# Kernel tuning notes

Measured on AMD Instinct MI355X. Metric: run time of the kernel, lower is better.

Reference implementation:

```python
import jax, jax.numpy as jnp
import numpy as np

N = 65536      # total nodes
D = 256        # score_dim
E = 128        # embed_dim
H = 8          # num_heads
HID = 256      # MLP hidden width
G = 128        # number of graphs (segments)


def setup_inputs() -> dict:
    key = jax.random.key(0)
    ks = jax.random.split(key, 16)
    w = lambda k, shape, s=0.02: jax.random.normal(k, shape, jnp.float32) * s
    return {
        "score_matrix": jax.random.normal(ks[0], (N, D), jnp.float32),
        "x": jax.random.normal(ks[1], (N, D), jnp.float32),  # unused by forward (as in source)
        "batch": jnp.sort(jax.random.randint(ks[2], (N,), 0, G)),
        "pos": jax.random.normal(ks[3], (1, D), jnp.float32),
        "para": jax.random.normal(ks[4], (1, E), jnp.float32),
        # stacked per-head MLP weights (q, k, v): in_dim->256->embed_dim
        "Wq1": w(ks[5], (H, D, HID)), "bq1": jnp.zeros((H, HID), jnp.float32),
        "Wq2": w(ks[6], (H, HID, E)), "bq2": jnp.zeros((H, E), jnp.float32),
        "Wk1": w(ks[7], (H, D, HID)), "bk1": jnp.zeros((H, HID), jnp.float32),
        "Wk2": w(ks[8], (H, HID, E)), "bk2": jnp.zeros((H, E), jnp.float32),
        "Wv1": w(ks[9], (H, D, HID)), "bv1": jnp.zeros((H, HID), jnp.float32),
        "Wv2": w(ks[10], (H, HID, E)), "bv2": jnp.zeros((H, E), jnp.float32),
        # out MLP: (H*E)->256->E
        "Wo1": w(ks[11], (H * E, HID)), "bo1": jnp.zeros((HID,), jnp.float32),
        "Wo2": w(ks[12], (HID, E)), "bo2": jnp.zeros((E,), jnp.float32),
    }


def _head_mlp(xs, W1, b1, W2, b2):
    # xs: [N, D]; W1: [H, D, HID]; W2: [H, HID, E] -> [N, H, E]
    h = jax.nn.relu(jnp.einsum('nd,hdk->nhk', xs, W1) + b1)
    return jnp.einsum('nhk,hke->nhe', h, W2) + b2


def _segment_softmax(src, idx, num_seg):
    # grouped softmax along axis 0 (matches torch scatter_max/scatter_add version)
    m = jax.ops.segment_max(src, idx, num_segments=num_seg)
    ex = jnp.exp(src - m[idx])
    den = jax.ops.segment_sum(ex, idx, num_segments=num_seg)[idx] + 1e-16
    return ex / den


def reference(score_matrix, x, batch, pos, para,
              Wq1, bq1, Wq2, bq2, Wk1, bk1, Wk2, bk2, Wv1, bv1, Wv2, bv2,
              Wo1, bo1, Wo2, bo2):
    sm = score_matrix + pos                                  # [N, D]
    q = _head_mlp(sm, Wq1, bq1, Wq2, bq2)                    # [N, H, E]
    k = _head_mlp(sm, Wk1, bk1, Wk2, bk2)                    # [N, H, E]
    v = _head_mlp(sm, Wv1, bv1, Wv2, bv2)                    # [N, H, E]
    scores = jnp.einsum('nhe,nge->nhg', q, k) / np.float32(np.sqrt(E))  # [N, H, H]
    aw = _segment_softmax(scores, batch, G)                  # [N, H, H]
    s = jnp.einsum('nhg,nge->nhe', aw, v).reshape(sm.shape[0], H * E)   # [N, H*E]
    out = jax.nn.relu(s @ Wo1 + bo1) @ Wo2 + bo2             # [N, E]
    return out + para
```

## Files before the change

kernel.cpp:

```cpp
#include <hip/hip_runtime.h>

#define N_NODES 65536
#define NSEG    128

using s16x8 = __attribute__((ext_vector_type(8))) short;
using s16x4 = __attribute__((ext_vector_type(4))) short;
using f32x4 = __attribute__((ext_vector_type(4))) float;

__device__ __forceinline__ float bf2f(unsigned short s) {
    union { unsigned u; float f; } x; x.u = ((unsigned)s) << 16; return x.f;
}
__device__ __forceinline__ short f2bf(float f) {
    union { float f; unsigned u; } x; x.f = f;
    unsigned r = x.u + 0x7FFFu + ((x.u >> 16) & 1u);
    return (short)(r >> 16);
}
__device__ __forceinline__ void gload_lds16(const void* g, void* lds) {
    __builtin_amdgcn_global_load_lds((const __attribute__((address_space(1))) void*)g,
                                     (__attribute__((address_space(3))) void*)lds, 16, 0, 0);
}


__global__ void prep_sm_kernel(const float* __restrict__ score, const float* __restrict__ pos,
                               short* __restrict__ sm) {
    int i = blockIdx.x * blockDim.x + threadIdx.x;
    int base = i * 4;
    f32x4 s = __builtin_nontemporal_load((const f32x4*)(score + base));
    f32x4 p = *(const f32x4*)(pos + (base & 255));
    s16x4 o;
#pragma unroll
    for (int j = 0; j < 4; ++j) o[j] = f2bf(s[j] + p[j]);
    *(s16x4*)(sm + base) = o;
}

__global__ void transpose_all_kernel(const float* __restrict__ Wq1, const float* __restrict__ Wk1,
                                     const float* __restrict__ Wv1, const float* __restrict__ Wq2,
                                     const float* __restrict__ Wk2, const float* __restrict__ Wv2,
                                     const float* __restrict__ Wo1, const float* __restrict__ Wo2,
                                     short* __restrict__ W1T, short* __restrict__ W2T,
                                     short* __restrict__ Wo1T, short* __restrict__ Wo2T) {
    int t = blockIdx.x;
    const float* in; short* out; int R, C, tx, ty;
    if (t < 1536) {
        int u = t >> 6, rem = t & 63;
        const float* s = (u < 8) ? Wq1 : (u < 16) ? Wk1 : Wv1;
        in = s + (long)(u & 7) * 65536; out = W1T + (long)u * 65536;
        R = 256; C = 256; tx = rem & 7; ty = rem >> 3;
    } else if (t < 2304) {
        int t2 = t - 1536, u = t2 >> 5, rem = t2 & 31;
        const float* s = (u < 8) ? Wq2 : (u < 16) ? Wk2 : Wv2;
        in = s + (long)(u & 7) * 32768; out = W2T + (long)u * 32768;
        R = 256; C = 128; tx = rem & 3; ty = rem >> 2;
    } else if (t < 2560) {
        int t3 = t - 2304;
        in = Wo1; out = Wo1T; R = 1024; C = 256; tx = t3 & 7; ty = t3 >> 3;
    } else {
        int t4 = t - 2560;
        in = Wo2; out = Wo2T; R = 256; C = 128; tx = t4 & 3; ty = t4 >> 2;
    }
    __shared__ float tbuf[32][33];
    const int c0 = tx * 32, r0 = ty * 32;
    const int lx = threadIdx.x & 31, ly = threadIdx.x >> 5;
#pragma unroll
    for (int i = 0; i < 32; i += 8)
        tbuf[ly + i][lx] = in[(long)(r0 + ly + i) * C + c0 + lx];
    __syncthreads();
#pragma unroll
    for (int i = 0; i < 32; i += 8)
        out[(long)(c0 + ly + i) * R + r0 + lx] = f2bf(tbuf[lx][ly + i]);
}

__global__ void prep_small_kernel(const float* __restrict__ bq1, const float* __restrict__ bk1,
                                  const float* __restrict__ bv1, const float* __restrict__ bq2,
                                  const float* __restrict__ bk2, const float* __restrict__ bv2,
                                  const float* __restrict__ bo2, const float* __restrict__ para,
                                  float* __restrict__ b1cat, float* __restrict__ b2cat,
                                  float* __restrict__ bo2p) {
    int i = blockIdx.x * blockDim.x + threadIdx.x;
    if (i < 6144) {
        int u = i >> 8, j = i & 255;
        const float* s = (u < 8) ? (bq1 + u * 256 + j)
                       : (u < 16) ? (bk1 + (u - 8) * 256 + j)
                                  : (bv1 + (u - 16) * 256 + j);
        b1cat[i] = *s;
    } else if (i < 9216) {
        int ii = i - 6144;
        int u = ii >> 7, j = ii & 127;
        const float* s = (u < 8) ? (bq2 + u * 128 + j)
                       : (u < 16) ? (bk2 + (u - 8) * 128 + j)
                                  : (bv2 + (u - 16) * 128 + j);
        b2cat[ii] = *s;
    } else if (i < 9344) {
        int e = i - 9216;
        bo2p[e] = bo2[e] + para[e];
    }
}

template <bool OUTBF16>
__global__ __launch_bounds__(512, 2)
void fused_mlp(const short* __restrict__ A, int lda,
               const short* __restrict__ B1, long b1_ustride,
               const float* __restrict__ bias1, int bias1_ustride,
               const short* __restrict__ B2, long b2_ustride,
               const float* __restrict__ bias2, int bias2_ustride,
               void* __restrict__ Cv, int ldc, long c_ustride, int K1) {
    const int u = blockIdx.y;
    B1    += (long)u * b1_ustride;
    bias1 += (long)u * bias1_ustride;
    B2    += (long)u * b2_ustride;
    bias2 += (long)u * bias2_ustride;

    __shared__ __align__(16) short lds[24576];
    short* Bs = lds;
    short* As = lds + 8192;
    short* hs = lds + 8192;

    const int tid = threadIdx.x, lane = tid & 63, wave = tid >> 6;
    const int wm = wave >> 2;
    const int wn = wave & 3;
    const int brow = blockIdx.x * 128;

    const int lrow = lane >> 3;
    const int schk = ((lane & 7) ^ lrow) * 8;
    const int nkt1 = K1 >> 6;
    const int l15 = lane & 15, lq = lane >> 4;

    f32x4 acc2[4][2];
#pragma unroll
    for (int i = 0; i < 4; ++i)
#pragma unroll
        for (int j = 0; j < 2; ++j) acc2[i][j] = (f32x4){0.f, 0.f, 0.f, 0.f};

    for (int p = 0; p < 2; ++p) {
        f32x4 acc1[4][2];
#pragma unroll
        for (int i = 0; i < 4; ++i)
#pragma unroll
            for (int j = 0; j < 2; ++j) acc1[i][j] = (f32x4){0.f, 0.f, 0.f, 0.f};

        for (int kt = 0; kt < nkt1; ++kt) {
            __syncthreads();
            const int ko = kt * 64;
#pragma unroll
            for (int i = 0; i < 2; ++i) {
                int cch = wave * 2 + i;
                int r = cch * 8 + lrow;
                gload_lds16(A  + (long)(brow + r) * lda + ko + schk, &As[cch * 512]);
                gload_lds16(B1 + (long)(p * 128 + r) * K1 + ko + schk, &Bs[cch * 512]);
            }
            __syncthreads();
#pragma unroll
            for (int kk = 0; kk < 2; ++kk) {
                const int slot = (((kk * 4) + lq) ^ (lane & 7)) * 8;
                s16x8 af[4], bfv[2];
#pragma unroll
                for (int i = 0; i < 4; ++i)
                    af[i] = *(const s16x8*)&As[(wm * 64 + i * 16 + l15) * 64 + slot];
#pragma unroll
                for (int j = 0; j < 2; ++j)
                    bfv[j] = *(const s16x8*)&Bs[(wn * 32 + j * 16 + l15) * 64 + slot];
#pragma unroll
                for (int i = 0; i < 4; ++i)
#pragma unroll
                    for (int j = 0; j < 2; ++j)
                        acc1[i][j] = __builtin_amdgcn_mfma_f32_16x16x32_bf16(bfv[j], af[i], acc1[i][j], 0, 0, 0);
            }
        }

        __syncthreads();

#pragma unroll
        for (int i = 0; i < 2; ++i) {
            int cch = wave * 2 + i;
            int r = cch * 8 + lrow;
            gload_lds16(B2 + (long)r * 256 + p * 128 + schk, &Bs[cch * 512]);
        }

        {
            const int cbq = lq << 2;
#pragma unroll
            for (int j = 0; j < 2; ++j) {
                int cb = wn * 32 + j * 16 + cbq;
                f32x4 bv = *(const f32x4*)(bias1 + p * 128 + cb);
#pragma unroll
                for (int i = 0; i < 4; ++i) {
                    int node = wm * 64 + i * 16 + l15;
                    s16x4 hv;
#pragma unroll
                    for (int r = 0; r < 4; ++r)
                        hv[r] = f2bf(fmaxf(acc1[i][j][r] + bv[r], 0.f));
                    *(s16x4*)&hs[node * 128 + (((cb >> 3) ^ (node & 7)) << 3) + (cb & 7)] = hv;
                }
            }
        }

#pragma unroll
        for (int kt2 = 0; kt2 < 2; ++kt2) {
            __syncthreads();
#pragma unroll
            for (int kk = 0; kk < 2; ++kk) {
                const int slotb = (((kk * 4) + lq) ^ (lane & 7)) * 8;
                s16x8 hf[4], wf[2];
#pragma unroll
                for (int i = 0; i < 4; ++i) {
                    int row = wm * 64 + i * 16 + l15;
                    int c = kt2 * 8 + kk * 4 + lq;
                    hf[i] = *(const s16x8*)&hs[row * 128 + ((c ^ (row & 7)) << 3)];
                }
#pragma unroll
                for (int j = 0; j < 2; ++j)
                    wf[j] = *(const s16x8*)&Bs[(wn * 32 + j * 16 + l15) * 64 + slotb];
#pragma unroll
                for (int i = 0; i < 4; ++i)
#pragma unroll
                    for (int j = 0; j < 2; ++j)
                        acc2[i][j] = __builtin_amdgcn_mfma_f32_16x16x32_bf16(wf[j], hf[i], acc2[i][j], 0, 0, 0);
            }
            if (kt2 == 0) {
                __syncthreads();
#pragma unroll
                for (int i = 0; i < 2; ++i) {
                    int cch = wave * 2 + i;
                    int r = cch * 8 + lrow;
                    gload_lds16(B2 + (long)r * 256 + p * 128 + 64 + schk, &Bs[cch * 512]);
                }
            }
        }
    }

    const int cbq = lq << 2;
    if (OUTBF16) {
        __syncthreads();
        short* Cs = hs;
#pragma unroll
        for (int j = 0; j < 2; ++j) {
            int cb = wn * 32 + j * 16 + cbq;
            f32x4 bv = *(const f32x4*)(bias2 + cb);
#pragma unroll
            for (int i = 0; i < 4; ++i) {
                int node = wm * 64 + i * 16 + l15;
                s16x4 ov;
#pragma unroll
                for (int r = 0; r < 4; ++r) ov[r] = f2bf(acc2[i][j][r] + bv[r]);
                *(s16x4*)&Cs[node * 128 + (((cb >> 3) ^ (node & 7)) << 3) + (cb & 7)] = ov;
            }
        }
        __syncthreads();
        short* cbase = (short*)Cv + u * c_ustride + (long)brow * ldc;
#pragma unroll
        for (int p8 = 0; p8 < 4; ++p8) {
            int g = tid + p8 * 512;
            int row = g >> 4, ck = g & 15;
            s16x8 val = *(const s16x8*)&Cs[row * 128 + ((ck ^ (row & 7)) * 8)];
            *(s16x8*)(cbase + (long)row * ldc + ck * 8) = val;
        }
    } else {
        float* cbase = (float*)Cv + u * c_ustride;
#pragma unroll
        for (int j = 0; j < 2; ++j) {
            int cb = wn * 32 + j * 16 + cbq;
            f32x4 bv = *(const f32x4*)(bias2 + cb);
#pragma unroll
            for (int i = 0; i < 4; ++i) {
                int node = wm * 64 + i * 16 + l15;
                f32x4 o;
#pragma unroll
                for (int r = 0; r < 4; ++r) o[r] = acc2[i][j][r] + bv[r];
                *(f32x4*)&cbase[(long)(brow + node) * ldc + cb] = o;
            }
        }
    }
}

__global__ __launch_bounds__(512, 2)
void fused_mlp2(const short* __restrict__ A, int lda,
                const short* __restrict__ B1,
                const float* __restrict__ bias1,
                const short* __restrict__ B2,
                const float* __restrict__ bias2,
                short* __restrict__ Cv, int ldc) {
    const int u = blockIdx.y;
    B1    += (long)u * 65536;
    bias1 += u * 256;
    B2    += (long)u * 32768;
    bias2 += u * 128;

    __shared__ __align__(16) short lds[24576];
    short* Ws  = lds;
    short* Bp0 = lds + 8192;
    short* Bp1 = lds + 16384;
    short* hs  = lds + 8192;

    const int tid = threadIdx.x, lane = tid & 63, wave = tid >> 6;
    const int wm = wave >> 2, wn = wave & 3;
    const int brow = blockIdx.x * 128;
    const int lrow = lane >> 3;
    const int schk = ((lane & 7) ^ lrow) * 8;
    const int l15 = lane & 15, lq = lane >> 4;
    const int cch0 = wave * 2, cch1 = cch0 + 1;
    const int ar0 = cch0 * 8 + lrow, ar1 = cch1 * 8 + lrow;

    f32x4 acc1[2][4][2];
    f32x4 acc2[4][2];
#pragma unroll
    for (int i = 0; i < 4; ++i)
#pragma unroll
        for (int j = 0; j < 2; ++j) {
            acc1[0][i][j] = (f32x4){0.f, 0.f, 0.f, 0.f};
            acc1[1][i][j] = (f32x4){0.f, 0.f, 0.f, 0.f};
            acc2[i][j]    = (f32x4){0.f, 0.f, 0.f, 0.f};
        }

    for (int kt = 0; kt < 4; ++kt) {
        __syncthreads();
        const int ko = kt * 64;
        gload_lds16(A + (long)(brow + ar0) * lda + ko + schk, &Ws[cch0 * 512]);
        gload_lds16(A + (long)(brow + ar1) * lda + ko + schk, &Ws[cch1 * 512]);
        gload_lds16(B1 + (long)ar0 * 256 + ko + schk, &Bp0[cch0 * 512]);
        gload_lds16(B1 + (long)ar1 * 256 + ko + schk, &Bp0[cch1 * 512]);
        gload_lds16(B1 + (long)(128 + ar0) * 256 + ko + schk, &Bp1[cch0 * 512]);
        gload_lds16(B1 + (long)(128 + ar1) * 256 + ko + schk, &Bp1[cch1 * 512]);
        __syncthreads();
#pragma unroll
        for (int kk = 0; kk < 2; ++kk) {
            const int slot = (((kk * 4) + lq) ^ (lane & 7)) * 8;
            s16x8 af[4], b0[2], b1v[2];
#pragma unroll
            for (int i = 0; i < 4; ++i)
                af[i] = *(const s16x8*)&Ws[(wm * 64 + i * 16 + l15) * 64 + slot];
#pragma unroll
            for (int j = 0; j < 2; ++j) {
                b0[j]  = *(const s16x8*)&Bp0[(wn * 32 + j * 16 + l15) * 64 + slot];
                b1v[j] = *(const s16x8*)&Bp1[(wn * 32 + j * 16 + l15) * 64 + slot];
            }
#pragma unroll
            for (int i = 0; i < 4; ++i)
#pragma unroll
                for (int j = 0; j < 2; ++j) {
                    acc1[0][i][j] = __builtin_amdgcn_mfma_f32_16x16x32_bf16(b0[j],  af[i], acc1[0][i][j], 0, 0, 0);
                    acc1[1][i][j] = __builtin_amdgcn_mfma_f32_16x16x32_bf16(b1v[j], af[i], acc1[1][i][j], 0, 0, 0);
                }
        }
    }

    __syncthreads();

    const int cbq = lq << 2;
#pragma unroll
    for (int p = 0; p < 2; ++p) {
        gload_lds16(B2 + (long)ar0 * 256 + p * 128 + schk, &Ws[cch0 * 512]);
        gload_lds16(B2 + (long)ar1 * 256 + p * 128 + schk, &Ws[cch1 * 512]);

#pragma unroll
        for (int j = 0; j < 2; ++j) {
            int cb = wn * 32 + j * 16 + cbq;
            f32x4 bv = *(const f32x4*)(bias1 + p * 128 + cb);
#pragma unroll
            for (int i = 0; i < 4; ++i) {
                int node = wm * 64 + i * 16 + l15;
                s16x4 hv;
#pragma unroll
                for (int r = 0; r < 4; ++r)
                    hv[r] = f2bf(fmaxf(acc1[p][i][j][r] + bv[r], 0.f));
                *(s16x4*)&hs[node * 128 + (((cb >> 3) ^ (node & 7)) << 3) + (cb & 7)] = hv;
            }
        }
        __syncthreads();

#pragma unroll
        for (int kt2 = 0; kt2 < 2; ++kt2) {
#pragma unroll
            for (int kk = 0; kk < 2; ++kk) {
                const int slotb = (((kk * 4) + lq) ^ (lane & 7)) * 8;
                s16x8 hf[4], wf[2];
#pragma unroll
                for (int i = 0; i < 4; ++i) {
                    int row = wm * 64 + i * 16 + l15;
                    int c = kt2 * 8 + kk * 4 + lq;
                    hf[i] = *(const s16x8*)&hs[row * 128 + ((c ^ (row & 7)) << 3)];
                }
#pragma unroll
                for (int j = 0; j < 2; ++j)
                    wf[j] = *(const s16x8*)&Ws[(wn * 32 + j * 16 + l15) * 64 + slotb];
#pragma unroll
                for (int i = 0; i < 4; ++i)
#pragma unroll
                    for (int j = 0; j < 2; ++j)
                        acc2[i][j] = __builtin_amdgcn_mfma_f32_16x16x32_bf16(wf[j], hf[i], acc2[i][j], 0, 0, 0);
            }
            if (kt2 == 0) {
                __syncthreads();
                gload_lds16(B2 + (long)ar0 * 256 + p * 128 + 64 + schk, &Ws[cch0 * 512]);
                gload_lds16(B2 + (long)ar1 * 256 + p * 128 + 64 + schk, &Ws[cch1 * 512]);
                __syncthreads();
            }
        }
        __syncthreads();
    }

    short* Cs = hs;
#pragma unroll
    for (int j = 0; j < 2; ++j) {
        int cb = wn * 32 + j * 16 + cbq;
        f32x4 bv = *(const f32x4*)(bias2 + cb);
#pragma unroll
        for (int i = 0; i < 4; ++i) {
            int node = wm * 64 + i * 16 + l15;
            s16x4 ov;
#pragma unroll
            for (int r = 0; r < 4; ++r) ov[r] = f2bf(acc2[i][j][r] + bv[r]);
            *(s16x4*)&Cs[node * 128 + (((cb >> 3) ^ (node & 7)) << 3) + (cb & 7)] = ov;
        }
    }
    __syncthreads();
    short* cbase = Cv + (long)u * 128 + (long)brow * ldc;
#pragma unroll
    for (int p8 = 0; p8 < 4; ++p8) {
        int g = tid + p8 * 512;
        int row = g >> 4, ck = g & 15;
        s16x8 val = *(const s16x8*)&Cs[row * 128 + ((ck ^ (row & 7)) * 8)];
        *(s16x8*)(cbase + (long)row * ldc + ck * 8) = val;
    }
}


__global__ void scores_mfma_kernel(const short* __restrict__ qk, float* __restrict__ scores,
                                   int nc) {
    const int lane = threadIdx.x & 63;
    int gw = (blockIdx.x * blockDim.x + threadIdx.x) >> 6;
    int nw = (gridDim.x * blockDim.x) >> 6;
    const int npairs = nc >> 1;
    const int r = lane & 15, ks = lane >> 4;
    for (int p = gw; p < npairs; p += nw) {
        const long n0 = (long)p * 2;
        const short* qp = qk + (n0 + (r >> 3)) * 2048 + (r & 7) * 128 + ks * 8;
        const short* kp = qp + 1024;
        f32x4 acc = (f32x4){0.f, 0.f, 0.f, 0.f};
#pragma unroll
        for (int kt = 0; kt < 4; ++kt) {
            s16x8 a = *(const s16x8*)(qp + kt * 32);
            s16x8 b = *(const s16x8*)(kp + kt * 32);
            acc = __builtin_amdgcn_mfma_f32_16x16x32_bf16(a, b, acc, 0, 0, 0);
        }
        const int c = lane & 15, rr0 = (lane >> 4) * 4;
        if ((rr0 >> 3) == (c >> 3)) {
            float* o = scores + (n0 + (rr0 >> 3)) * 64 + (c & 7);
#pragma unroll
            for (int reg = 0; reg < 4; ++reg)
                o[((rr0 & 7) + reg) * 8] = acc[reg] * 0.08838834764831845f;
        }
    }
}

__global__ void segstats1_kernel(const float* __restrict__ scores, const int* __restrict__ batch,
                                 float* __restrict__ pm, float* __restrict__ ps) {
    const int g = blockIdx.x, sl = blockIdx.y;
    int lo = 0, hi = N_NODES;
    while (lo < hi) { int mid = (lo + hi) >> 1; if (batch[mid] < g) lo = mid + 1; else hi = mid; }
    const int start = lo;
    hi = N_NODES;
    while (lo < hi) { int mid = (lo + hi) >> 1; if (batch[mid] <= g) lo = mid + 1; else hi = mid; }
    const int end = lo;
    const int len = end - start;
    const int s0 = start + (len * sl) / 8;
    const int s1 = start + (len * (sl + 1)) / 8;

    const int e = threadIdx.x & 63, sub = threadIdx.x >> 6;
    __shared__ float red[4][64];
    float m = -1e30f;
    for (int n = s0 + sub; n < s1; n += 4)
        m = fmaxf(m, scores[(long)n * 64 + e]);
    red[sub][e] = m;
    __syncthreads();
    m = fmaxf(fmaxf(red[0][e], red[1][e]), fmaxf(red[2][e], red[3][e]));
    __syncthreads();
    float s = 0.f;
    for (int n = s0 + sub; n < s1; n += 4)
        s += expf(scores[(long)n * 64 + e] - m);
    red[sub][e] = s;
    __syncthreads();
    if (sub == 0) {
        int idx = (g * 8 + sl) * 64 + e;
        pm[idx] = m;
        ps[idx] = red[0][e] + red[1][e] + red[2][e] + red[3][e];
    }
}

__global__ void segstats2_kernel(const float* __restrict__ pm, const float* __restrict__ ps,
                                 float* __restrict__ segm, float* __restrict__ segdinv) {
    const int g = blockIdx.x, e = threadIdx.x;
    float M = -1e30f;
#pragma unroll
    for (int sl = 0; sl < 8; ++sl)
        M = fmaxf(M, pm[(g * 8 + sl) * 64 + e]);
    float den = 1e-16f;
#pragma unroll
    for (int sl = 0; sl < 8; ++sl) {
        int idx = (g * 8 + sl) * 64 + e;
        den += ps[idx] * expf(pm[idx] - M);
    }
    segm[g * 64 + e]    = M;
    segdinv[g * 64 + e] = 1.f / den;
}

__global__ void pv_kernel(const short* __restrict__ v, short* __restrict__ sout,
                          const float* __restrict__ scores, const int* __restrict__ batch,
                          const float* __restrict__ segm, const float* __restrict__ segdinv,
                          int n0) {
    __shared__ float aw[16][64];
    const int t = threadIdx.x;
    const int nodeL0 = blockIdx.x * 16;
    {
        int j0 = t * 4;
        int nl = j0 >> 6, e0 = j0 & 63;
        int n = n0 + nodeL0 + nl;
        int b = batch[n];
        f32x4 sc = *(const f32x4*)(scores + (long)n * 64 + e0);
#pragma unroll
        for (int i = 0; i < 4; ++i)
            aw[nl][e0 + i] = expf(sc[i] - segm[b * 64 + e0 + i]) * segdinv[b * 64 + e0 + i];
    }
    __syncthreads();
    const int nl = t >> 4;
    const int ec = (t & 15) * 8;
    const long nloc = nodeL0 + nl;
    const short* vp = v + nloc * 1024 + ec;
    float acc[8][8];
#pragma unroll
    for (int h = 0; h < 8; ++h)
#pragma unroll
        for (int j = 0; j < 8; ++j) acc[h][j] = 0.f;
#pragma unroll
    for (int g = 0; g < 8; ++g) {
        s16x8 vv = *(const s16x8*)(vp + g * 128);
        float vf[8];
#pragma unroll
        for (int j = 0; j < 8; ++j) vf[j] = bf2f((unsigned short)vv[j]);
#pragma unroll
        for (int h = 0; h < 8; ++h) {
            float wgt = aw[nl][h * 8 + g];
#pragma unroll
            for (int j = 0; j < 8; ++j) acc[h][j] += wgt * vf[j];
        }
    }
#pragma unroll
    for (int h = 0; h < 8; ++h) {
        s16x8 o;
#pragma unroll
        for (int j = 0; j < 8; ++j) o[j] = f2bf(acc[h][j]);
        *(s16x8*)(sout + nloc * 1024 + h * 128 + ec) = o;
    }
}


extern "C" void kernel_launch(void* const* d_in, const int* in_sizes, int n_in,
                              void* d_out, int out_size, void* d_ws, size_t ws_size,
                              hipStream_t stream) {
    const float* score = (const float*)d_in[0];
    const int*   batch = (const int*)d_in[2];
    const float* pos   = (const float*)d_in[3];
    const float* para  = (const float*)d_in[4];
    const float* Wq1 = (const float*)d_in[5];
    const float* bq1 = (const float*)d_in[6];
    const float* Wq2 = (const float*)d_in[7];
    const float* bq2 = (const float*)d_in[8];
    const float* Wk1 = (const float*)d_in[9];
    const float* bk1 = (const float*)d_in[10];
    const float* Wk2 = (const float*)d_in[11];
    const float* bk2 = (const float*)d_in[12];
    const float* Wv1 = (const float*)d_in[13];
    const float* bv1 = (const float*)d_in[14];
    const float* Wv2 = (const float*)d_in[15];
    const float* bv2 = (const float*)d_in[16];
    const float* Wo1 = (const float*)d_in[17];
    const float* bo1 = (const float*)d_in[18];
    const float* Wo2 = (const float*)d_in[19];
    const float* bo2 = (const float*)d_in[20];
    float* out = (float*)d_out;
    (void)in_sizes; (void)n_in; (void)out_size;

    char* w = (char*)d_ws;
    short* sm     = (short*)w; w += (size_t)N_NODES * 256 * 2;
    float* scoresb= (float*)w; w += (size_t)N_NODES * 64 * 4;
    short* W1T    = (short*)w; w += (size_t)24 * 256 * 256 * 2;
    short* W2T    = (short*)w; w += (size_t)24 * 128 * 256 * 2;
    short* Wo1T   = (short*)w; w += (size_t)256 * 1024 * 2;
    short* Wo2T   = (short*)w; w += (size_t)128 * 256 * 2;
    float* b1cat  = (float*)w; w += 6144 * 4;
    float* b2cat  = (float*)w; w += 3072 * 4;
    float* bo2p   = (float*)w; w += 1024;
    float* segm   = (float*)w; w += 8192 * 4;
    float* segdi  = (float*)w; w += 8192 * 4;
    float* pm     = (float*)w; w += 65536 * 4;
    float* ps     = (float*)w; w += 65536 * 4;
    size_t persist = (size_t)(w - (char*)d_ws);
    size_t area = ws_size - persist;

    int NC = 32768;
    while (NC > 1024 && (size_t)NC * 4096 > area) NC >>= 1;
    const int nchunks = N_NODES / NC;
    short* X = (short*)w;

    prep_sm_kernel<<<N_NODES * 256 / 4 / 256, 256, 0, stream>>>(score, pos, sm);
    transpose_all_kernel<<<2592, 256, 0, stream>>>(Wq1, Wk1, Wv1, Wq2, Wk2, Wv2, Wo1, Wo2,
                                                   W1T, W2T, Wo1T, Wo2T);
    prep_small_kernel<<<37, 256, 0, stream>>>(bq1, bk1, bv1, bq2, bk2, bv2, bo2, para,
                                              b1cat, b2cat, bo2p);

    for (int c = 0; c < nchunks; ++c) {
        const int n0 = c * NC;
        if (c & 1) {
            fused_mlp2<<<dim3(NC / 128, 16), 512, 0, stream>>>(
                sm + (size_t)n0 * 256, 256, W1T, b1cat, W2T, b2cat, X, 2048);
        } else {
            fused_mlp<true><<<dim3(NC / 128, 16), 512, 0, stream>>>(
                sm + (size_t)n0 * 256, 256, W1T, 65536, b1cat, 256,
                W2T, 32768, b2cat, 128, X, 2048, 128, 256);
        }
        scores_mfma_kernel<<<NC / 8, 256, 0, stream>>>(X, scoresb + (size_t)n0 * 64, NC);
    }

    segstats1_kernel<<<dim3(NSEG, 8), 256, 0, stream>>>(scoresb, batch, pm, ps);
    segstats2_kernel<<<NSEG, 64, 0, stream>>>(pm, ps, segm, segdi);

    const size_t sfull_bytes = (size_t)N_NODES * 2048;
    if (area >= sfull_bytes + (size_t)4096 * 2048) {
        int NCB = 16384;
        while ((size_t)NCB * 2048 + sfull_bytes > area) NCB >>= 1;
        short* sfull = (short*)w;
        short* v     = sfull + (size_t)N_NODES * 1024;
        for (int c = 0; c < N_NODES / NCB; ++c) {
            const int n0 = c * NCB;
            fused_mlp<true><<<dim3(NCB / 128, 8), 512, 0, stream>>>(
                sm + (size_t)n0 * 256, 256, W1T + 16 * 65536, 65536, b1cat + 16 * 256, 256,
                W2T + 16 * 32768, 32768, b2cat + 16 * 128, 128, v, 1024, 128, 256);
            pv_kernel<<<NCB / 16, 256, 0, stream>>>(v, sfull + (size_t)n0 * 1024,
                                                    scoresb, batch, segm, segdi, n0);
        }
        fused_mlp<false><<<dim3(N_NODES / 128, 1), 512, 0, stream>>>(
            sfull, 1024, Wo1T, 0, bo1, 0, Wo2T, 0, bo2p, 0, out, 128, 0, 1024);
    } else {
        int NCB = 32768;
        while (NCB > 1024 && (size_t)NCB * 4096 > area) NCB >>= 1;
        short* v = (short*)w;
        short* s = v + (size_t)NCB * 1024;
        for (int c = 0; c < N_NODES / NCB; ++c) {
            const int n0 = c * NCB;
            fused_mlp<true><<<dim3(NCB / 128, 8), 512, 0, stream>>>(
                sm + (size_t)n0 * 256, 256, W1T + 16 * 65536, 65536, b1cat + 16 * 256, 256,
                W2T + 16 * 32768, 32768, b2cat + 16 * 128, 128, v, 1024, 128, 256);
            pv_kernel<<<NCB / 16, 256, 0, stream>>>(v, s, scoresb, batch, segm, segdi, n0);
            fused_mlp<false><<<dim3(NCB / 128, 1), 512, 0, stream>>>(
                s, 1024, Wo1T, 0, bo1, 0, Wo2T, 0, bo2p, 0,
                out + (size_t)n0 * 128, 128, 0, 1024);
        }
    }
}
```

Measured before the change: 647.3 us.

## Stream MLP weights from global into registers and use packed bf16 conversion

```diff
diff --git a/kernel.cpp b/kernel.cpp
--- a/kernel.cpp
+++ b/kernel.cpp
@@ -6,6 +6,7 @@
 using s16x8 = __attribute__((ext_vector_type(8))) short;
 using s16x4 = __attribute__((ext_vector_type(4))) short;
 using f32x4 = __attribute__((ext_vector_type(4))) float;
+using u32x2 = __attribute__((ext_vector_type(2))) unsigned;
 
 __device__ __forceinline__ float bf2f(unsigned short s) {
     union { unsigned u; float f; } x; x.u = ((unsigned)s) << 16; return x.f;
@@ -14,6 +15,11 @@
     union { float f; unsigned u; } x; x.f = f;
     unsigned r = x.u + 0x7FFFu + ((x.u >> 16) & 1u);
     return (short)(r >> 16);
+}
+__device__ __forceinline__ unsigned cvtpk(float a, float b) {
+    unsigned r;
+    asm("v_cvt_pk_bf16_f32 %0, %1, %2" : "=v"(r) : "v"(a), "v"(b));
+    return r;
 }
 __device__ __forceinline__ void gload_lds16(const void* g, void* lds) {
     __builtin_amdgcn_global_load_lds((const __attribute__((address_space(1))) void*)g,
@@ -185,11 +191,12 @@
 #pragma unroll
                 for (int i = 0; i < 4; ++i) {
                     int node = wm * 64 + i * 16 + l15;
-                    s16x4 hv;
-#pragma unroll
-                    for (int r = 0; r < 4; ++r)
-                        hv[r] = f2bf(fmaxf(acc1[i][j][r] + bv[r], 0.f));
-                    *(s16x4*)&hs[node * 128 + (((cb >> 3) ^ (node & 7)) << 3) + (cb & 7)] = hv;
+                    float t0 = fmaxf(acc1[i][j][0] + bv[0], 0.f);
+                    float t1 = fmaxf(acc1[i][j][1] + bv[1], 0.f);
+                    float t2 = fmaxf(acc1[i][j][2] + bv[2], 0.f);
+                    float t3 = fmaxf(acc1[i][j][3] + bv[3], 0.f);
+                    u32x2 hw; hw[0] = cvtpk(t0, t1); hw[1] = cvtpk(t2, t3);
+                    *(u32x2*)&hs[node * 128 + (((cb >> 3) ^ (node & 7)) << 3) + (cb & 7)] = hw;
                 }
             }
         }
@@ -239,10 +246,10 @@
 #pragma unroll
             for (int i = 0; i < 4; ++i) {
                 int node = wm * 64 + i * 16 + l15;
-                s16x4 ov;
-#pragma unroll
-                for (int r = 0; r < 4; ++r) ov[r] = f2bf(acc2[i][j][r] + bv[r]);
-                *(s16x4*)&Cs[node * 128 + (((cb >> 3) ^ (node & 7)) << 3) + (cb & 7)] = ov;
+                u32x2 ow;
+                ow[0] = cvtpk(acc2[i][j][0] + bv[0], acc2[i][j][1] + bv[1]);
+                ow[1] = cvtpk(acc2[i][j][2] + bv[2], acc2[i][j][3] + bv[3]);
+                *(u32x2*)&Cs[node * 128 + (((cb >> 3) ^ (node & 7)) << 3) + (cb & 7)] = ow;
             }
         }
         __syncthreads();
@@ -272,154 +279,178 @@
     }
 }
 
+template <bool OUTBF16>
 __global__ __launch_bounds__(512, 2)
-void fused_mlp2(const short* __restrict__ A, int lda,
-                const short* __restrict__ B1,
-                const float* __restrict__ bias1,
-                const short* __restrict__ B2,
-                const float* __restrict__ bias2,
-                short* __restrict__ Cv, int ldc) {
+void fused_mlpB(const short* __restrict__ A, int lda,
+                const short* __restrict__ B1, long b1_ustride,
+                const float* __restrict__ bias1, int bias1_ustride,
+                const short* __restrict__ B2, long b2_ustride,
+                const float* __restrict__ bias2, int bias2_ustride,
+                void* __restrict__ Cv, int ldc, long c_ustride, int K1) {
     const int u = blockIdx.y;
-    B1    += (long)u * 65536;
-    bias1 += u * 256;
-    B2    += (long)u * 32768;
-    bias2 += u * 128;
+    B1    += (long)u * b1_ustride;
+    bias1 += (long)u * bias1_ustride;
+    B2    += (long)u * b2_ustride;
+    bias2 += (long)u * bias2_ustride;
 
     __shared__ __align__(16) short lds[24576];
-    short* Ws  = lds;
-    short* Bp0 = lds + 8192;
-    short* Bp1 = lds + 16384;
-    short* hs  = lds + 8192;
+    short* Aa = lds;
+    short* Ab = lds + 4096;
+    short* hs = lds + 8192;
 
     const int tid = threadIdx.x, lane = tid & 63, wave = tid >> 6;
     const int wm = wave >> 2, wn = wave & 3;
     const int brow = blockIdx.x * 128;
-    const int lrow = lane >> 3;
-    const int schk = ((lane & 7) ^ lrow) * 8;
     const int l15 = lane & 15, lq = lane >> 4;
-    const int cch0 = wave * 2, cch1 = cch0 + 1;
-    const int ar0 = cch0 * 8 + lrow, ar1 = cch1 * 8 + lrow;
-
-    f32x4 acc1[2][4][2];
+    const int nkt = K1 >> 5;
+
+    const int arow  = wave * 16 + (lane >> 2);
+    const int aslog = ((lane & 3) ^ ((lane >> 2) & 3)) * 8;
+    const int slotA = (lq ^ (l15 & 3)) * 8;
+
+#define STAGE_A(ko, dst) \
+    gload_lds16(A + (long)(brow + arow) * lda + (ko) + aslog, (dst) + wave * 512)
+
     f32x4 acc2[4][2];
 #pragma unroll
     for (int i = 0; i < 4; ++i)
 #pragma unroll
-        for (int j = 0; j < 2; ++j) {
-            acc1[0][i][j] = (f32x4){0.f, 0.f, 0.f, 0.f};
-            acc1[1][i][j] = (f32x4){0.f, 0.f, 0.f, 0.f};
-            acc2[i][j]    = (f32x4){0.f, 0.f, 0.f, 0.f};
-        }
-
-    for (int kt = 0; kt < 4; ++kt) {
+        for (int j = 0; j < 2; ++j) acc2[i][j] = (f32x4){0.f, 0.f, 0.f, 0.f};
+
+    STAGE_A(0, Aa);
+
+    for (int p = 0; p < 2; ++p) {
+        f32x4 acc1[4][2];
+#pragma unroll
+        for (int i = 0; i < 4; ++i)
+#pragma unroll
+            for (int j = 0; j < 2; ++j) acc1[i][j] = (f32x4){0.f, 0.f, 0.f, 0.f};
+
+        const short* B1p = B1 + (long)(p * 128 + wn * 32 + l15) * K1;
+
+        for (int kt = 0; kt < nkt; kt += 2) {
+            __syncthreads();
+            if (kt + 1 < nkt) STAGE_A((kt + 1) * 32, Ab);
+            {
+                s16x8 af[4], bfv[2];
+#pragma unroll
+                for (int i = 0; i < 4; ++i)
+                    af[i] = *(const s16x8*)&Aa[(wm * 64 + i * 16 + l15) * 32 + slotA];
+#pragma unroll
+                for (int j = 0; j < 2; ++j)
+                    bfv[j] = *(const s16x8*)(B1p + (long)j * 16 * K1 + kt * 32 + lq * 8);
+#pragma unroll
+                for (int i = 0; i < 4; ++i)
+#pragma unroll
+                    for (int j = 0; j < 2; ++j)
+                        acc1[i][j] = __builtin_amdgcn_mfma_f32_16x16x32_bf16(bfv[j], af[i], acc1[i][j], 0, 0, 0);
+            }
+            __syncthreads();
+            if (kt + 2 < nkt) STAGE_A((kt + 2) * 32, Aa);
+            {
+                s16x8 af[4], bfv[2];
+#pragma unroll
+                for (int i = 0; i < 4; ++i)
+                    af[i] = *(const s16x8*)&Ab[(wm * 64 + i * 16 + l15) * 32 + slotA];
+#pragma unroll
+                for (int j = 0; j < 2; ++j)
+                    bfv[j] = *(const s16x8*)(B1p + (long)j * 16 * K1 + (kt + 1) * 32 + lq * 8);
+#pragma unroll
+                for (int i = 0; i < 4; ++i)
+#pragma unroll
+                    for (int j = 0; j < 2; ++j)
+                        acc1[i][j] = __builtin_amdgcn_mfma_f32_16x16x32_bf16(bfv[j], af[i], acc1[i][j], 0, 0, 0);
+            }
+        }
+
+        if (p == 0) STAGE_A(0, Aa);
+
+        {
+            const int cbq = lq << 2;
+#pragma unroll
+            for (int j = 0; j < 2; ++j) {
+                int cb = wn * 32 + j * 16 + cbq;
+                f32x4 bv = *(const f32x4*)(bias1 + p * 128 + cb);
+#pragma unroll
+                for (int i = 0; i < 4; ++i) {
+                    int node = wm * 64 + i * 16 + l15;
+                    float t0 = fmaxf(acc1[i][j][0] + bv[0], 0.f);
+                    float t1 = fmaxf(acc1[i][j][1] + bv[1], 0.f);
+                    float t2 = fmaxf(acc1[i][j][2] + bv[2], 0.f);
+                    float t3 = fmaxf(acc1[i][j][3] + bv[3], 0.f);
+                    u32x2 hw; hw[0] = cvtpk(t0, t1); hw[1] = cvtpk(t2, t3);
+                    *(u32x2*)&hs[node * 128 + (((cb >> 3) ^ (node & 7)) << 3) + (cb & 7)] = hw;
+                }
+            }
+        }
         __syncthreads();
-        const int ko = kt * 64;
-        gload_lds16(A + (long)(brow + ar0) * lda + ko + schk, &Ws[cch0 * 512]);
-        gload_lds16(A + (long)(brow + ar1) * lda + ko + schk, &Ws[cch1 * 512]);
-        gload_lds16(B1 + (long)ar0 * 256 + ko + schk, &Bp0[cch0 * 512]);
-        gload_lds16(B1 + (long)ar1 * 256 + ko + schk, &Bp0[cch1 * 512]);
-        gload_lds16(B1 + (long)(128 + ar0) * 256 + ko + schk, &Bp1[cch0 * 512]);
-        gload_lds16(B1 + (long)(128 + ar1) * 256 + ko + schk, &Bp1[cch1 * 512]);
+
+        const short* B2p = B2 + (long)(wn * 32 + l15) * 256 + p * 128;
+#pragma unroll
+        for (int kt2 = 0; kt2 < 2; ++kt2) {
+#pragma unroll
+            for (int kk = 0; kk < 2; ++kk) {
+                const int c = kt2 * 8 + kk * 4 + lq;
+                s16x8 hf[4], wf[2];
+#pragma unroll
+                for (int i = 0; i < 4; ++i) {
+                    int row = wm * 64 + i * 16 + l15;
+                    hf[i] = *(const s16x8*)&hs[row * 128 + ((c ^ (row & 7)) << 3)];
+                }
+#pragma unroll
+                for (int j = 0; j < 2; ++j)
+                    wf[j] = *(const s16x8*)(B2p + (long)j * 16 * 256 + kt2 * 64 + kk * 32 + lq * 8);
+#pragma unroll
+                for (int i = 0; i < 4; ++i)
+#pragma unroll
+                    for (int j = 0; j < 2; ++j)
+                        acc2[i][j] = __builtin_amdgcn_mfma_f32_16x16x32_bf16(wf[j], hf[i], acc2[i][j], 0, 0, 0);
+            }
+        }
         __syncthreads();
-#pragma unroll
-        for (int kk = 0; kk < 2; ++kk) {
-            const int slot = (((kk * 4) + lq) ^ (lane & 7)) * 8;
-            s16x8 af[4], b0[2], b1v[2];
-#pragma unroll
-            for (int i = 0; i < 4; ++i)
-                af[i] = *(const s16x8*)&Ws[(wm * 64 + i * 16 + l15) * 64 + slot];
-#pragma unroll
-            for (int j = 0; j < 2; ++j) {
-                b0[j]  = *(const s16x8*)&Bp0[(wn * 32 + j * 16 + l15) * 64 + slot];
-                b1v[j] = *(const s16x8*)&Bp1[(wn * 32 + j * 16 + l15) * 64 + slot];
-            }
-#pragma unroll
-            for (int i = 0; i < 4; ++i)
-#pragma unroll
-                for (int j = 0; j < 2; ++j) {
-                    acc1[0][i][j] = __builtin_amdgcn_mfma_f32_16x16x32_bf16(b0[j],  af[i], acc1[0][i][j], 0, 0, 0);
-                    acc1[1][i][j] = __builtin_amdgcn_mfma_f32_16x16x32_bf16(b1v[j], af[i], acc1[1][i][j], 0, 0, 0);
-                }
-        }
-    }
-
-    __syncthreads();
+    }
+#undef STAGE_A
 
     const int cbq = lq << 2;
-#pragma unroll
-    for (int p = 0; p < 2; ++p) {
-        gload_lds16(B2 + (long)ar0 * 256 + p * 128 + schk, &Ws[cch0 * 512]);
-        gload_lds16(B2 + (long)ar1 * 256 + p * 128 + schk, &Ws[cch1 * 512]);
-
+    if (OUTBF16) {
+        short* Cs = hs;
 #pragma unroll
         for (int j = 0; j < 2; ++j) {
             int cb = wn * 32 + j * 16 + cbq;
-            f32x4 bv = *(const f32x4*)(bias1 + p * 128 + cb);
+            f32x4 bv = *(const f32x4*)(bias2 + cb);
 #pragma unroll
             for (int i = 0; i < 4; ++i) {
                 int node = wm * 64 + i * 16 + l15;
-                s16x4 hv;
-#pragma unroll
-                for (int r = 0; r < 4; ++r)
-                    hv[r] = f2bf(fmaxf(acc1[p][i][j][r] + bv[r], 0.f));
-                *(s16x4*)&hs[node * 128 + (((cb >> 3) ^ (node & 7)) << 3) + (cb & 7)] = hv;
+                u32x2 ow;
+                ow[0] = cvtpk(acc2[i][j][0] + bv[0], acc2[i][j][1] + bv[1]);
+                ow[1] = cvtpk(acc2[i][j][2] + bv[2], acc2[i][j][3] + bv[3]);
+                *(u32x2*)&Cs[node * 128 + (((cb >> 3) ^ (node & 7)) << 3) + (cb & 7)] = ow;
             }
         }
         __syncthreads();
-
-#pragma unroll
-        for (int kt2 = 0; kt2 < 2; ++kt2) {
-#pragma unroll
-            for (int kk = 0; kk < 2; ++kk) {
-                const int slotb = (((kk * 4) + lq) ^ (lane & 7)) * 8;
-                s16x8 hf[4], wf[2];
-#pragma unroll
-                for (int i = 0; i < 4; ++i) {
-                    int row = wm * 64 + i * 16 + l15;
-                    int c = kt2 * 8 + kk * 4 + lq;
-                    hf[i] = *(const s16x8*)&hs[row * 128 + ((c ^ (row & 7)) << 3)];
-                }
-#pragma unroll
-                for (int j = 0; j < 2; ++j)
-                    wf[j] = *(const s16x8*)&Ws[(wn * 32 + j * 16 + l15) * 64 + slotb];
-#pragma unroll
-                for (int i = 0; i < 4; ++i)
-#pragma unroll
-                    for (int j = 0; j < 2; ++j)
-                        acc2[i][j] = __builtin_amdgcn_mfma_f32_16x16x32_bf16(wf[j], hf[i], acc2[i][j], 0, 0, 0);
-            }
-            if (kt2 == 0) {
-                __syncthreads();
-                gload_lds16(B2 + (long)ar0 * 256 + p * 128 + 64 + schk, &Ws[cch0 * 512]);
-                gload_lds16(B2 + (long)ar1 * 256 + p * 128 + 64 + schk, &Ws[cch1 * 512]);
-                __syncthreads();
-            }
-        }
-        __syncthreads();
-    }
-
-    short* Cs = hs;
-#pragma unroll
-    for (int j = 0; j < 2; ++j) {
-        int cb = wn * 32 + j * 16 + cbq;
-        f32x4 bv = *(const f32x4*)(bias2 + cb);
-#pragma unroll
-        for (int i = 0; i < 4; ++i) {
-            int node = wm * 64 + i * 16 + l15;
-            s16x4 ov;
-#pragma unroll
-            for (int r = 0; r < 4; ++r) ov[r] = f2bf(acc2[i][j][r] + bv[r]);
-            *(s16x4*)&Cs[node * 128 + (((cb >> 3) ^ (node & 7)) << 3) + (cb & 7)] = ov;
-        }
-    }
-    __syncthreads();
-    short* cbase = Cv + (long)u * 128 + (long)brow * ldc;
-#pragma unroll
-    for (int p8 = 0; p8 < 4; ++p8) {
-        int g = tid + p8 * 512;
-        int row = g >> 4, ck = g & 15;
-        s16x8 val = *(const s16x8*)&Cs[row * 128 + ((ck ^ (row & 7)) * 8)];
-        *(s16x8*)(cbase + (long)row * ldc + ck * 8) = val;
+        short* cbase = (short*)Cv + u * c_ustride + (long)brow * ldc;
+#pragma unroll
+        for (int p8 = 0; p8 < 4; ++p8) {
+            int g = tid + p8 * 512;
+            int row = g >> 4, ck = g & 15;
+            s16x8 val = *(const s16x8*)&Cs[row * 128 + ((ck ^ (row & 7)) * 8)];
+            *(s16x8*)(cbase + (long)row * ldc + ck * 8) = val;
+        }
+    } else {
+        float* cbase = (float*)Cv + u * c_ustride;
+#pragma unroll
+        for (int j = 0; j < 2; ++j) {
+            int cb = wn * 32 + j * 16 + cbq;
+            f32x4 bv = *(const f32x4*)(bias2 + cb);
+#pragma unroll
+            for (int i = 0; i < 4; ++i) {
+                int node = wm * 64 + i * 16 + l15;
+                f32x4 o;
+#pragma unroll
+                for (int r = 0; r < 4; ++r) o[r] = acc2[i][j][r] + bv[r];
+                *(f32x4*)&cbase[(long)(brow + node) * ldc + cb] = o;
+            }
+        }
     }
 }
 
@@ -545,10 +576,11 @@
     }
 #pragma unroll
     for (int h = 0; h < 8; ++h) {
-        s16x8 o;
-#pragma unroll
-        for (int j = 0; j < 8; ++j) o[j] = f2bf(acc[h][j]);
-        *(s16x8*)(sout + nloc * 1024 + h * 128 + ec) = o;
+        union { s16x8 vv; unsigned uu[4]; } o;
+#pragma unroll
+        for (int jj = 0; jj < 4; ++jj)
+            o.uu[jj] = cvtpk(acc[h][2 * jj], acc[h][2 * jj + 1]);
+        *(s16x8*)(sout + nloc * 1024 + h * 128 + ec) = o.vv;
     }
 }
 
@@ -610,8 +642,9 @@
     for (int c = 0; c < nchunks; ++c) {
         const int n0 = c * NC;
         if (c & 1) {
-            fused_mlp2<<<dim3(NC / 128, 16), 512, 0, stream>>>(
-                sm + (size_t)n0 * 256, 256, W1T, b1cat, W2T, b2cat, X, 2048);
+            fused_mlpB<true><<<dim3(NC / 128, 16), 512, 0, stream>>>(
+                sm + (size_t)n0 * 256, 256, W1T, 65536, b1cat, 256,
+                W2T, 32768, b2cat, 128, X, 2048, 128, 256);
         } else {
             fused_mlp<true><<<dim3(NC / 128, 16), 512, 0, stream>>>(
                 sm + (size_t)n0 * 256, 256, W1T, 65536, b1cat, 256,
```

After: 671.8 us. 3.8% more time.
